# Kernel tuning notes

Measured on AMD Instinct MI355X. Metric: run time of the kernel, lower is better.

## Reference

```python
import jax, jax.numpy as jnp
import numpy as np

T = 2048            # flattened tokens (vLLM style)
D = 4096            # hidden_size
NSSM = 128          # ssm_state_size
K = 4               # conv kernel size
G = 8               # n_groups
H = 128             # mamba_num_heads
P = 64              # mamba_head_dim
INTER = H * P       # 8192 = expand * hidden_size
CONV_DIM = INTER + 2 * G * NSSM   # 10240 (x, B, C share the conv)
PROJ = INTER + CONV_DIM + H       # 18560 (z, xBC, dt)
Q = 128             # SSD chunk size
EPS = 1e-5


def setup_inputs() -> dict:
    key = jax.random.key(0)
    ks = jax.random.split(key, 9)
    s = 0.02
    return {
        "hidden_states": jax.random.normal(ks[0], (T, D), jnp.float32),
        "residual": jax.random.normal(ks[1], (T, D), jnp.float32),
        "norm_w": jnp.ones((D,), jnp.float32),
        "in_proj_w": jax.random.normal(ks[2], (PROJ, D), jnp.float32) * s,
        "conv_w": jax.random.normal(ks[3], (CONV_DIM, K), jnp.float32) * 0.2,
        "conv_b": jax.random.normal(ks[4], (CONV_DIM,), jnp.float32) * 0.1,
        "A_log": jnp.log(jax.random.uniform(ks[5], (H,), jnp.float32, 1.0, 16.0)),
        "D_res": jax.random.normal(ks[6], (H,), jnp.float32) * 0.5 + 1.0,
        "dt_bias": jax.random.normal(ks[7], (H,), jnp.float32) * 0.5,
        "gn_w": jnp.ones((INTER,), jnp.float32),
        "out_proj_w": jax.random.normal(ks[8], (D, INTER), jnp.float32) * s,
    }


def _forward(hidden_states, residual, norm_w, in_proj_w, conv_w, conv_b,
             A_log, D_res, dt_bias, gn_w, out_proj_w):
    # ---- fused add + RMSNorm (vLLM RMSNorm(hidden, residual)) ----
    resid = hidden_states + residual
    hs = resid * jax.lax.rsqrt(jnp.mean(resid * resid, -1, keepdims=True) + EPS) * norm_w

    # ---- MambaMixer2 ----
    proj = hs @ in_proj_w.T                              # [T, PROJ]
    z, xBC, dt = jnp.split(proj, [INTER, INTER + CONV_DIM], axis=-1)

    # causal depthwise conv1d over time + SiLU
    xp = jnp.pad(xBC, ((K - 1, 0), (0, 0)))
    conv = conv_b + sum(conv_w[:, k] * xp[k:k + T] for k in range(K))
    xBC = jax.nn.silu(conv)

    x, B, C = jnp.split(xBC, [INTER, INTER + G * NSSM], axis=-1)
    x = x.reshape(T, H, P)
    Bh = jnp.repeat(B.reshape(T, G, NSSM), H // G, axis=1)   # [T,H,N]
    Ch = jnp.repeat(C.reshape(T, G, NSSM), H // G, axis=1)   # [T,H,N]

    dt = jax.nn.softplus(dt + dt_bias)                   # [T,H]
    A = -jnp.exp(A_log)                                  # [H] (negative)

    # ---- SSD chunked selective scan ----
    NC = T // Q
    a = (dt * A).reshape(NC, Q, H)                       # per-step log decay (<=0)
    cum = jnp.cumsum(a, axis=1)                          # inclusive cumsum, [NC,Q,H]
    Xd = (dt[:, :, None] * x).reshape(NC, Q, H, P)
    Bc = Bh.reshape(NC, Q, H, NSSM)
    Cc = Ch.reshape(NC, Q, H, NSSM)

    # intra-chunk: Y[i] = sum_{j<=i} (C_i.B_j) exp(cum_i-cum_j) Xd_j
    CB = jnp.einsum('cqhn,ckhn->chqk', Cc, Bc)
    cumT = cum.transpose(0, 2, 1)                        # [NC,H,Q]
    mask = jnp.tril(jnp.ones((Q, Q), bool))
    Lm = jnp.where(mask, jnp.exp(cumT[:, :, :, None] - cumT[:, :, None, :]), 0.0)
    Y = jnp.einsum('chqk,ckhp->cqhp', CB * Lm, Xd)

    # chunk-local end states, then scan states across chunks
    cum_end = cum[:, -1]                                 # [NC,H]
    decay_out = jnp.exp(cum_end[:, None] - cum)          # [NC,Q,H]
    S_loc = jnp.einsum('cqhn,cqh,cqhp->chnp', Bc, decay_out, Xd)
    chunk_decay = jnp.exp(cum_end)                       # [NC,H]

    def step(s, inp):
        dec, sl = inp
        return dec[:, None, None] * s + sl, s            # emit state BEFORE chunk

    _, S_prev = jax.lax.scan(step, jnp.zeros((H, NSSM, P), x.dtype),
                             (chunk_decay, S_loc))       # [NC,H,N,P]

    # inter-chunk contribution + skip connection D*x
    Y = Y + jnp.einsum('cqhn,cqh,chnp->cqhp', Cc, jnp.exp(cum), S_prev)
    y = Y.reshape(T, H, P) + D_res[None, :, None] * x

    # gated RMSNorm then out projection
    y = y.reshape(T, INTER) * jax.nn.silu(z)
    y = y * jax.lax.rsqrt(jnp.mean(y * y, -1, keepdims=True) + EPS) * gn_w
    return y @ out_proj_w.T, resid


def reference(hidden_states, residual, norm_w, in_proj_w, conv_w, conv_b,
              A_log, D_res, dt_bias, gn_w, out_proj_w):
    return _forward(hidden_states, residual, norm_w, in_proj_w, conv_w, conv_b,
                    A_log, D_res, dt_bias, gn_w, out_proj_w)
```

## Files before the change

### kernel.cpp

```cpp
#include <hip/hip_runtime.h>
#include <stdint.h>

typedef unsigned short u16;
typedef unsigned int   u32;
typedef float  f32x4  __attribute__((ext_vector_type(4)));
typedef __bf16 bf16x8 __attribute__((ext_vector_type(8)));
typedef u16    u16x4  __attribute__((ext_vector_type(4)));
typedef u16    u16x8  __attribute__((ext_vector_type(8)));

#define T_N     2048
#define D_N     4096
#define H_N     128
#define P_N     64
#define G_N     8
#define NS_N    128
#define INTER_N 8192
#define CONVD_N 10240
#define PROJ_N  18560
#define NGEMM_N 18432
#define NC_N    16

__device__ __forceinline__ float bf2f(u16 u){ u32 x = ((u32)u) << 16; return __builtin_bit_cast(float, x); }
__device__ __forceinline__ u16 f2bf(float f){
  u32 u = __builtin_bit_cast(u32, f);
  u += 0x7FFFu + ((u >> 16) & 1u);
  return (u16)(u >> 16);
}

__device__ __forceinline__ void gld_lds16(const void* g, void* lds){
  __builtin_amdgcn_global_load_lds(
      (const __attribute__((address_space(1))) void*)(uintptr_t)g,
      (__attribute__((address_space(3))) void*)(u32)(uintptr_t)lds,
      16, 0, 0);
}

__global__ __launch_bounds__(256)
void k_addnorm(const float* __restrict__ hin, const float* __restrict__ rin,
               const float* __restrict__ nw, float* __restrict__ resid,
               u16* __restrict__ hs16, float* __restrict__ rstd){
  __shared__ float red[4];
  const int row = blockIdx.x, tid = threadIdx.x;
  const size_t rb = (size_t)row * D_N;
  f32x4 s[4];
  float ss = 0.f;
  #pragma unroll
  for (int i = 0; i < 4; ++i){
    int c4 = tid + i*256;
    f32x4 a = *(const f32x4*)&hin[rb + (size_t)c4*4];
    f32x4 b = *(const f32x4*)&rin[rb + (size_t)c4*4];
    s[i] = a + b;
    *(f32x4*)&resid[rb + (size_t)c4*4] = s[i];
    ss += s[i][0]*s[i][0] + s[i][1]*s[i][1] + s[i][2]*s[i][2] + s[i][3]*s[i][3];
  }
  #pragma unroll
  for (int o = 32; o > 0; o >>= 1) ss += __shfl_down(ss, o, 64);
  if ((tid & 63) == 0) red[tid >> 6] = ss;
  __syncthreads();
  float tot = (red[0] + red[1]) + (red[2] + red[3]);
  float rs = rsqrtf(tot / (float)D_N + 1e-5f);
  if (tid == 0) rstd[row] = rs;
  #pragma unroll
  for (int i = 0; i < 4; ++i){
    int c4 = tid + i*256;
    f32x4 w = *(const f32x4*)&nw[(size_t)c4*4];
    u16x4 o = { f2bf(s[i][0]*rs*w[0]), f2bf(s[i][1]*rs*w[1]),
                f2bf(s[i][2]*rs*w[2]), f2bf(s[i][3]*rs*w[3]) };
    *(u16x4*)&hs16[rb + (size_t)c4*4] = o;
  }
}

__global__ void k_cvt(const float* __restrict__ in, u16* __restrict__ out, size_t n4){
  size_t i = (size_t)blockIdx.x * blockDim.x + threadIdx.x;
  size_t stride = (size_t)gridDim.x * blockDim.x;
  for (; i < n4; i += stride){
    f32x4 v = *(const f32x4*)&in[i*4];
    u16x4 o = { f2bf(v[0]), f2bf(v[1]), f2bf(v[2]), f2bf(v[3]) };
    *(u16x4*)&out[i*4] = o;
  }
}

__global__ __launch_bounds__(256)
void k_wdt(const float* __restrict__ W, const float* __restrict__ nw,
           float* __restrict__ Wn){
  __shared__ float lt[32][133];
  const int tid = threadIdx.x;
  const int d0 = blockIdx.x * 32;
  #pragma unroll
  for (int i = 0; i < 16; ++i){
    int h = i*8 + (tid >> 5);
    int d = tid & 31;
    lt[d][h] = W[(size_t)(INTER_N + CONVD_N + h)*D_N + d0 + d];
  }
  __syncthreads();
  #pragma unroll
  for (int i = 0; i < 4; ++i){
    int d = i*8 + (tid >> 5);
    int h4 = (tid & 31) * 4;
    float nwv = nw[d0 + d];
    f32x4 v = { lt[d][h4]*nwv, lt[d][h4+1]*nwv, lt[d][h4+2]*nwv, lt[d][h4+3]*nwv };
    *(f32x4*)&Wn[(size_t)(d0 + d)*128 + h4] = v;
  }
}

__global__ __launch_bounds__(256)
void k_dtgemm(const float* __restrict__ resid, const float* __restrict__ Wn,
              float* __restrict__ dtpart){
  __shared__ float lhs[16*128];
  const int tid = threadIdx.x;
  const int tb = blockIdx.x >> 3, ks = blockIdx.x & 7;
  const int t0 = tb * 16;
  const int k0 = ks * (D_N / 8);
  const int hcol = tid & 127, rh = tid >> 7;
  float acc[8] = {0,0,0,0,0,0,0,0};
  for (int kt = k0; kt < k0 + D_N/8; kt += 128){
    __syncthreads();
    #pragma unroll
    for (int it = 0; it < 2; ++it){
      int idx = it*256 + tid;
      int rr = idx >> 5, c4 = idx & 31;
      *(f32x4*)&lhs[rr*128 + c4*4] = *(const f32x4*)&resid[(size_t)(t0+rr)*D_N + kt + c4*4];
    }
    __syncthreads();
    #pragma unroll 4
    for (int kk4 = 0; kk4 < 32; ++kk4){
      f32x4 w4;
      #pragma unroll
      for (int j = 0; j < 4; ++j) w4[j] = Wn[(size_t)(kt + kk4*4 + j)*128 + hcol];
      #pragma unroll
      for (int j = 0; j < 8; ++j){
        f32x4 lv = *(const f32x4*)&lhs[(rh*8 + j)*128 + kk4*4];
        acc[j] += lv[0]*w4[0] + lv[1]*w4[1] + lv[2]*w4[2] + lv[3]*w4[3];
      }
    }
  }
  #pragma unroll
  for (int j = 0; j < 8; ++j){
    int t = t0 + rh*8 + j;
    dtpart[((size_t)ks*T_N + t)*128 + hcol] = acc[j];
  }
}

__global__ __launch_bounds__(256)
void k_dtsum(const float* __restrict__ dtpart, const float* __restrict__ rstd,
             const float* __restrict__ dt_bias, const float* __restrict__ A_log,
             float* __restrict__ dtv, float* __restrict__ dta){
  int idx = blockIdx.x*256 + threadIdx.x;
  int t = idx >> 7, h = idx & 127;
  float s = 0.f;
  #pragma unroll
  for (int k = 0; k < 8; ++k) s += dtpart[((size_t)k*T_N + t)*128 + h];
  float x = s * rstd[t] + dt_bias[h];
  float dv = (x > 20.f) ? x : log1pf(expf(x));
  dtv[idx] = dv;
  dta[idx] = dv * (-expf(A_log[h]));
}

__global__ void k_dtprep(const float* __restrict__ dta, float* __restrict__ cum,
                         float* __restrict__ cumend, float* __restrict__ dec){
  int c = blockIdx.x, h = threadIdx.x;
  float cm = 0.f;
  for (int q = 0; q < 128; ++q){
    size_t i = (size_t)(c*128 + q)*128 + h;
    cm += dta[i];
    cum[i] = cm;
  }
  cumend[c*128 + h] = cm;
  dec[c*128 + h] = expf(cm);
}

#define STA(BUF,HH,KT) gld_lds16(pA + (size_t)((HH)*32)*K + (size_t)(KT)*64, shb + (BUF)*BSZ + (HH)*4096 + tid*16)
#define STB(BUF,HH,KT) gld_lds16(pB + (size_t)((HH)*32)*K + (size_t)(KT)*64, shb + (BUF)*BSZ + 16384 + (HH)*4096 + tid*16)
#define VMWN do { asm volatile("s_waitcnt vmcnt(%0)" :: "n"(NF) : "memory"); __builtin_amdgcn_sched_barrier(0); } while(0)
#define RDA4(BUF, MOFF)                                                                 \
    bf16x8 a0 = *(const bf16x8*)(shb + (BUF)*BSZ + rdA + (MOFF)*2048 + sA0);            \
    bf16x8 a1 = *(const bf16x8*)(shb + (BUF)*BSZ + rdA + (MOFF)*2048 + sA1);            \
    bf16x8 a2 = *(const bf16x8*)(shb + (BUF)*BSZ + rdA + ((MOFF)+1)*2048 + sA0);        \
    bf16x8 a3 = *(const bf16x8*)(shb + (BUF)*BSZ + rdA + ((MOFF)+1)*2048 + sA1);
#define RDBALL(BUF, BB)                                                                 \
    _Pragma("unroll") for (int nn = 0; nn < NF; ++nn){                                  \
      BB[nn][0] = *(const bf16x8*)(shb + (BUF)*BSZ + rdB + nn*2048 + sA0);              \
      BB[nn][1] = *(const bf16x8*)(shb + (BUF)*BSZ + rdB + nn*2048 + sA1);              \
    }
#define MM24(MOFF, BB)                                                                  \
    _Pragma("unroll") for (int nn = 0; nn < NF; ++nn)                                   \
      acc[(MOFF)+0][nn] = __builtin_amdgcn_mfma_f32_16x16x32_bf16(a0, BB[nn][0], acc[(MOFF)+0][nn],0,0,0); \
    _Pragma("unroll") for (int nn = 0; nn < NF; ++nn)                                   \
      acc[(MOFF)+1][nn] = __builtin_amdgcn_mfma_f32_16x16x32_bf16(a2, BB[nn][0], acc[(MOFF)+1][nn],0,0,0); \
    _Pragma("unroll") for (int nn = 0; nn < NF; ++nn)                                   \
      acc[(MOFF)+0][nn] = __builtin_amdgcn_mfma_f32_16x16x32_bf16(a1, BB[nn][1], acc[(MOFF)+0][nn],0,0,0); \
    _Pragma("unroll") for (int nn = 0; nn < NF; ++nn)                                   \
      acc[(MOFF)+1][nn] = __builtin_amdgcn_mfma_f32_16x16x32_bf16(a3, BB[nn][1], acc[(MOFF)+1][nn],0,0,0);
#define ENDPH                                                                           \
    __builtin_amdgcn_s_setprio(0);                                                      \
    __builtin_amdgcn_s_barrier();                                                       \
    __builtin_amdgcn_sched_barrier(0);

template<int NF, typename OT>
__global__ __launch_bounds__(256, 2)
void k_gemmw(const u16* __restrict__ A, const u16* __restrict__ Bm,
             OT* __restrict__ C, int ldc, int K, int nkt){
  constexpr int BSZ = 16384 + NF*4096;
  __shared__ char shb[2*BSZ];
  const int tid = threadIdx.x, ln = tid & 63, wid = tid >> 6;
  const int wm = wid >> 1, wn = wid & 1;
  const int lr = ln & 15, lg = ln >> 4;

  const int gx = gridDim.x;
  const int mt = gridDim.y;
  const int lin = blockIdx.y * gx + blockIdx.x;
  const int xcd = lin & 7, sub = lin >> 3;
  const int ncx = gx >> 3;
  const int n_local = sub / mt;
  const int m_idx   = sub % mt;
  const int m0 = m_idx << 7;
  const int n0 = (xcd * ncx + n_local) * (NF*32);

  const int srow = tid >> 3;
  const int slog = ((tid & 7) ^ (srow & 7)) * 8;
  const u16* pA = A + (size_t)(m0 + srow)*K + slog;
  const u16* pB = Bm + (size_t)(n0 + srow)*K + slog;

  const int sA0 = (lg ^ (ln & 7)) << 4;
  const int sA1 = ((4 + lg) ^ (ln & 7)) << 4;
  const u32 rdA = wm*8192 + lr*128;
  const u32 rdB = 16384 + wn*(NF*2048) + lr*128;

  f32x4 acc[4][NF] = {};

  STA(0,0,0); STA(0,1,0); STA(0,2,0); STA(0,3,0);
  #pragma unroll
  for (int hh = 0; hh < NF; ++hh) STB(0, hh, 0);
  #pragma unroll
  for (int hh = 0; hh < NF; ++hh) STB(1, hh, 1);
  VMWN;
  __builtin_amdgcn_s_barrier();
  __builtin_amdgcn_sched_barrier(0);

  const int nit = nkt >> 1;
  #pragma unroll 1
  for (int it = 0; it < nit; ++it){
    const int t1 = 2*it + 1;
    int t2 = 2*it + 2; if (t2 >= nkt) t2 = 0;
    int t3 = 2*it + 3; if (t3 >= nkt) t3 = 1;
    bf16x8 bb0[NF][2], bb1[NF][2];
    { RDA4(0, 0) RDBALL(0, bb0)
      STA(1,0,t1); STA(1,1,t1); STA(1,2,t1); STA(1,3,t1);
      __builtin_amdgcn_s_setprio(1);
      MM24(0, bb0)
      ENDPH }
    { RDA4(0, 2)
      #pragma unroll
      for (int hh = 0; hh < NF; ++hh) STB(0, hh, t2);
      VMWN;
      __builtin_amdgcn_s_setprio(1);
      MM24(2, bb0)
      ENDPH }
    { RDA4(1, 0) RDBALL(1, bb1)
      STA(0,0,t2); STA(0,1,t2); STA(0,2,t2); STA(0,3,t2);
      __builtin_amdgcn_s_setprio(1);
      MM24(0, bb1)
      ENDPH }
    { RDA4(1, 2)
      #pragma unroll
      for (int hh = 0; hh < NF; ++hh) STB(1, hh, t3);
      VMWN;
      __builtin_amdgcn_s_setprio(1);
      MM24(2, bb1)
      ENDPH }
  }
  asm volatile("s_waitcnt vmcnt(0)" ::: "memory");

  const int crow = m0 + wm*64 + lg*4;
  const int ccol = n0 + wn*(NF*16) + lr;
  #pragma unroll
  for (int m = 0; m < 4; ++m)
    #pragma unroll
    for (int nn = 0; nn < NF; ++nn)
      #pragma unroll
      for (int r = 0; r < 4; ++r){
        float v = acc[m][nn][r];
        if constexpr (__is_same(OT, float))
          C[(size_t)(crow + m*16 + r)*ldc + ccol + nn*16] = v;
        else
          C[(size_t)(crow + m*16 + r)*ldc + ccol + nn*16] = f2bf(v);
      }
}

__global__ __launch_bounds__(256)
void k_conv(const u16* __restrict__ proj16, const float* __restrict__ cw,
            const float* __restrict__ cb, u16* __restrict__ x16,
            u16* __restrict__ B16, u16* __restrict__ C16){
  const int ch0 = blockIdx.x*2048 + threadIdx.x*8;
  const int tbase = blockIdx.y*16;
  f32x4 w[8]; float bias[8];
  #pragma unroll
  for (int j = 0; j < 8; ++j){
    w[j] = *(const f32x4*)&cw[(size_t)(ch0+j)*4];
    bias[j] = cb[ch0+j];
  }
  const u16* pcol = proj16 + INTER_N + ch0;
  float p0[8], p1[8], p2[8];
  if (tbase >= 3){
    u16x8 v0 = *(const u16x8*)&pcol[(size_t)(tbase-3)*PROJ_N];
    u16x8 v1 = *(const u16x8*)&pcol[(size_t)(tbase-2)*PROJ_N];
    u16x8 v2 = *(const u16x8*)&pcol[(size_t)(tbase-1)*PROJ_N];
    #pragma unroll
    for (int j = 0; j < 8; ++j){ p0[j]=bf2f(v0[j]); p1[j]=bf2f(v1[j]); p2[j]=bf2f(v2[j]); }
  } else {
    #pragma unroll
    for (int j = 0; j < 8; ++j){ p0[j]=0.f; p1[j]=0.f; p2[j]=0.f; }
  }
  u16* xdst = (ch0 < INTER_N) ? x16 + ch0
            : (ch0 < INTER_N + 1024) ? B16 + (ch0 - INTER_N)
            : C16 + (ch0 - INTER_N - 1024);
  const int dstride = (ch0 < INTER_N) ? INTER_N : 1024;
  #pragma unroll 2
  for (int i = 0; i < 16; ++i){
    int t = tbase + i;
    u16x8 cv = *(const u16x8*)&pcol[(size_t)t*PROJ_N];
    u16x8 o;
    #pragma unroll
    for (int j = 0; j < 8; ++j){
      float cur = bf2f(cv[j]);
      float a = bias[j] + w[j][0]*p0[j] + w[j][1]*p1[j] + w[j][2]*p2[j] + w[j][3]*cur;
      o[j] = f2bf(a / (1.f + __expf(-a)));
      p0[j] = p1[j]; p1[j] = p2[j]; p2[j] = cur;
    }
    *(u16x8*)&xdst[(size_t)t*dstride] = o;
  }
}

__global__ __launch_bounds__(512)
void k_ssda(const u16* __restrict__ B16, const u16* __restrict__ x16,
            const float* __restrict__ dtv, const float* __restrict__ cum,
            const float* __restrict__ cumend, u16* __restrict__ SlocT){
  __shared__ u16 lBdT[128*136];
  __shared__ u16 lXdT[64*136];
  __shared__ float lDec[128], lDt[128];
  const int tid = threadIdx.x, wid = tid >> 6, ln = tid & 63;
  const int c = blockIdx.x >> 7, h = blockIdx.x & 127, g = h >> 4;
  if (tid < 128){
    int t = c*128 + tid;
    lDec[tid] = __expf(cumend[c*128 + h] - cum[(size_t)t*128 + h]);
    lDt[tid]  = dtv[(size_t)t*128 + h];
  }
  __syncthreads();
  for (int it = 0; it < 32; ++it){
    int idx = it*512 + tid;
    int q = idx >> 7, n = idx & 127;
    float bv = bf2f(B16[(size_t)(c*128 + q)*1024 + g*128 + n]) * lDec[q];
    lBdT[n*136 + q] = f2bf(bv);
  }
  for (int it = 0; it < 16; ++it){
    int idx = it*512 + tid;
    int q = idx >> 6, p = idx & 63;
    float xv = bf2f(x16[(size_t)(c*128 + q)*INTER_N + h*64 + p]) * lDt[q];
    lXdT[p*136 + q] = f2bf(xv);
  }
  __syncthreads();
  const int wr = wid >> 1, wc = wid & 1;
  const int kofs = (ln >> 4) << 3;
  f32x4 acc[2][2] = {};
  #pragma unroll
  for (int ks = 0; ks < 4; ++ks){
    bf16x8 a[2], b[2];
    #pragma unroll
    for (int m = 0; m < 2; ++m) a[m] = *(const bf16x8*)&lBdT[(wr*32 + m*16 + (ln & 15))*136 + ks*32 + kofs];
    #pragma unroll
    for (int n = 0; n < 2; ++n) b[n] = *(const bf16x8*)&lXdT[(wc*32 + n*16 + (ln & 15))*136 + ks*32 + kofs];
    #pragma unroll
    for (int m = 0; m < 2; ++m)
      #pragma unroll
      for (int n = 0; n < 2; ++n)
        acc[m][n] = __builtin_amdgcn_mfma_f32_16x16x32_bf16(a[m], b[n], acc[m][n], 0, 0, 0);
  }
  const size_t base = (size_t)(c*128 + h) * 8192;
  #pragma unroll
  for (int m = 0; m < 2; ++m)
    #pragma unroll
    for (int n = 0; n < 2; ++n){
      int p  = wc*32 + n*16 + (ln & 15);
      int nn = wr*32 + m*16 + ((ln >> 4) << 2);
      u16x4 o = { f2bf(acc[m][n][0]), f2bf(acc[m][n][1]), f2bf(acc[m][n][2]), f2bf(acc[m][n][3]) };
      *(u16x4*)&SlocT[base + (size_t)p*128 + nn] = o;
    }
}

__global__ __launch_bounds__(256)
void k_scan(const u16* __restrict__ SlocT, const float* __restrict__ dec,
            u16* __restrict__ SprevT){
  int idx = blockIdx.x*256 + threadIdx.x;
  int h = idx >> 10, p = (idx >> 4) & 63, n8 = (idx & 15)*8;
  float s[8] = {};
  for (int c = 0; c < NC_N; ++c){
    size_t off = (size_t)(c*128 + h)*8192 + (size_t)p*128 + n8;
    u16x8 o;
    #pragma unroll
    for (int j = 0; j < 8; ++j) o[j] = f2bf(s[j]);
    *(u16x8*)&SprevT[off] = o;
    u16x8 sl = *(const u16x8*)&SlocT[off];
    float d = dec[c*128 + h];
    #pragma unroll
    for (int j = 0; j < 8; ++j) s[j] = d*s[j] + bf2f(sl[j]);
  }
}

__global__ __launch_bounds__(512)
void k_ssdb(const u16* __restrict__ C16, const u16* __restrict__ B16g,
            const u16* __restrict__ x16, const float* __restrict__ dtv,
            const float* __restrict__ cum, const u16* __restrict__ SprevT,
            const u16* __restrict__ proj16, const float* __restrict__ Dres,
            u16* __restrict__ yg16){
  __shared__ u16 lC[128*136];
  __shared__ u16 lBP[128*136];
  __shared__ u16 lXdT[64*136];
  __shared__ float lCum[128], lDt[128];
  const int tid = threadIdx.x, wid = tid >> 6, ln = tid & 63;
  const int c = blockIdx.x >> 7, h = blockIdx.x & 127, g = h >> 4;
  if (tid < 128){
    int t = c*128 + tid;
    lCum[tid] = cum[(size_t)t*128 + h];
    lDt[tid]  = dtv[(size_t)t*128 + h];
  }
  __syncthreads();
  #pragma unroll
  for (int it = 0; it < 4; ++it){
    int idx = it*512 + tid;
    int q = idx >> 4, n8 = (idx & 15) << 3;
    size_t gi = (size_t)(c*128 + q)*1024 + g*128 + n8;
    *(u16x8*)&lC[q*136 + n8]  = *(const u16x8*)&C16[gi];
    *(u16x8*)&lBP[q*136 + n8] = *(const u16x8*)&B16g[gi];
  }
  for (int it = 0; it < 16; ++it){
    int idx = it*512 + tid;
    int q = idx >> 6, p = idx & 63;
    lXdT[p*136 + q] = f2bf(bf2f(x16[(size_t)(c*128 + q)*INTER_N + h*64 + p]) * lDt[q]);
  }
  __syncthreads();
  const int kofs = (ln >> 4) << 3;
  {
    const int wr = wid >> 2, wc = wid & 3;
    f32x4 cb[4][2] = {};
    #pragma unroll
    for (int ks = 0; ks < 4; ++ks){
      bf16x8 a[4], b[2];
      #pragma unroll
      for (int m = 0; m < 4; ++m) a[m] = *(const bf16x8*)&lC[(wr*64 + m*16 + (ln & 15))*136 + ks*32 + kofs];
      #pragma unroll
      for (int n = 0; n < 2; ++n) b[n] = *(const bf16x8*)&lBP[(wc*32 + n*16 + (ln & 15))*136 + ks*32 + kofs];
      #pragma unroll
      for (int m = 0; m < 4; ++m)
        #pragma unroll
        for (int n = 0; n < 2; ++n)
          cb[m][n] = __builtin_amdgcn_mfma_f32_16x16x32_bf16(a[m], b[n], cb[m][n], 0, 0, 0);
    }
    __syncthreads();
    #pragma unroll
    for (int m = 0; m < 4; ++m)
      #pragma unroll
      for (int n = 0; n < 2; ++n){
        int kcol = (wid & 3)*32 + n*16 + (ln & 15);
        float ck = lCum[kcol];
        #pragma unroll
        for (int r = 0; r < 4; ++r){
          int q = (wid >> 2)*64 + m*16 + ((ln >> 4) << 2) + r;
          float v = (kcol <= q) ? cb[m][n][r] * __expf(lCum[q] - ck) : 0.f;
          lBP[q*136 + kcol] = f2bf(v);
        }
      }
  }
  __syncthreads();
  const int yr = wid >> 1, yc = wid & 1;
  f32x4 y1[2][2] = {}, y2[2][2] = {};
  const size_t spbase = (size_t)(c*128 + h) * 8192;
  #pragma unroll
  for (int ks = 0; ks < 4; ++ks){
    bf16x8 ap[2], acf[2], bx[2], bs[2];
    #pragma unroll
    for (int m = 0; m < 2; ++m){
      int qr = yr*32 + m*16 + (ln & 15);
      ap[m]  = *(const bf16x8*)&lBP[qr*136 + ks*32 + kofs];
      acf[m] = *(const bf16x8*)&lC [qr*136 + ks*32 + kofs];
    }
    #pragma unroll
    for (int n = 0; n < 2; ++n){
      int p = yc*32 + n*16 + (ln & 15);
      bx[n] = *(const bf16x8*)&lXdT[p*136 + ks*32 + kofs];
      bs[n] = *(const bf16x8*)&SprevT[spbase + (size_t)p*128 + ks*32 + kofs];
    }
    #pragma unroll
    for (int m = 0; m < 2; ++m)
      #pragma unroll
      for (int n = 0; n < 2; ++n){
        y1[m][n] = __builtin_amdgcn_mfma_f32_16x16x32_bf16(ap[m],  bx[n], y1[m][n], 0, 0, 0);
        y2[m][n] = __builtin_amdgcn_mfma_f32_16x16x32_bf16(acf[m], bs[n], y2[m][n], 0, 0, 0);
      }
  }
  const float dh = Dres[h];
  #pragma unroll
  for (int m = 0; m < 2; ++m)
    #pragma unroll
    for (int r = 0; r < 4; ++r){
      int q = yr*32 + m*16 + ((ln >> 4) << 2) + r;
      float eq = __expf(lCum[q]);
      size_t t = (size_t)(c*128 + q);
      #pragma unroll
      for (int n = 0; n < 2; ++n){
        int p = yc*32 + n*16 + (ln & 15);
        int chn = h*64 + p;
        float xv = bf2f(x16[t*INTER_N + chn]);
        float zv = bf2f(proj16[t*PROJ_N + chn]);
        float yv = y1[m][n][r] + eq*y2[m][n][r] + dh*xv;
        float sg = zv / (1.f + __expf(-zv));
        yg16[t*INTER_N + chn] = f2bf(yv * sg);
      }
    }
}

__global__ __launch_bounds__(256)
void k_gnorm(const u16* __restrict__ yg, const float* __restrict__ gnw,
             u16* __restrict__ yn16){
  __shared__ float red[4];
  const int row = blockIdx.x, tid = threadIdx.x;
  const u16* rp = yg + (size_t)row * INTER_N;
  u16x8 v[4];
  float ss = 0.f;
  #pragma unroll
  for (int i = 0; i < 4; ++i){
    v[i] = *(const u16x8*)&rp[(size_t)(tid + i*256)*8];
    #pragma unroll
    for (int j = 0; j < 8; ++j){ float f = bf2f(v[i][j]); ss += f*f; }
  }
  #pragma unroll
  for (int o = 32; o > 0; o >>= 1) ss += __shfl_down(ss, o, 64);
  if ((tid & 63) == 0) red[tid >> 6] = ss;
  __syncthreads();
  float tot = (red[0] + red[1]) + (red[2] + red[3]);
  float sc = rsqrtf(tot / (float)INTER_N + 1e-5f);
  #pragma unroll
  for (int i = 0; i < 4; ++i){
    int c8 = (tid + i*256)*8;
    u16x8 o;
    #pragma unroll
    for (int j = 0; j < 8; ++j)
      o[j] = f2bf(bf2f(v[i][j]) * sc * gnw[c8 + j]);
    *(u16x8*)&yn16[(size_t)row*INTER_N + c8] = o;
  }
}

extern "C" void kernel_launch(void* const* d_in, const int* in_sizes, int n_in,
                              void* d_out, int out_size, void* d_ws, size_t ws_size,
                              hipStream_t stream){
  (void)in_sizes; (void)n_in; (void)out_size;
  const float* hs_in     = (const float*)d_in[0];
  const float* res_in    = (const float*)d_in[1];
  const float* norm_w    = (const float*)d_in[2];
  const float* in_proj_w = (const float*)d_in[3];
  const float* conv_w    = (const float*)d_in[4];
  const float* conv_b    = (const float*)d_in[5];
  const float* A_log     = (const float*)d_in[6];
  const float* D_res     = (const float*)d_in[7];
  const float* dt_bias   = (const float*)d_in[8];
  const float* gn_w      = (const float*)d_in[9];
  const float* out_proj_w= (const float*)d_in[10];

  float* out0      = (float*)d_out;
  float* resid_out = out0 + (size_t)T_N * D_N;

  char* ws = (char*)d_ws;
  const size_t o_hs16   = 0;
  const size_t o_Win16  = 16777216;
  const size_t o_Wout16 = 168820736;
  const size_t o_proj   = 235929600;
  const size_t o_Wn     = 387973120;
  const size_t o_dtv    = 391118848;
  const size_t o_cum    = 392167424;
  const size_t o_cumend = 393216000;
  const size_t o_dec    = 393224192;
  const size_t o_rstd   = 393232384;
  const size_t o_x16    = 393240576;
  const size_t o_B16    = 426795008;
  const size_t o_C16    = 430989312;
  const size_t o_SlocT  = 435183616;
  const size_t o_SprevT = 468738048;
  const size_t o_yn16   = 502292480;
  const size_t WS_NEED  = 535846912;
  if (ws_size < WS_NEED) return;

  u16*   hs16   = (u16*)  (ws + o_hs16);
  u16*   Win16  = (u16*)  (ws + o_Win16);
  u16*   Wout16 = (u16*)  (ws + o_Wout16);
  u16*   proj16 = (u16*)  (ws + o_proj);
  float* Wn     = (float*)(ws + o_Wn);
  float* dtpart = (float*)(ws + o_proj);
  float* dta    = (float*)(ws + o_proj + (16u<<20));
  float* dtv    = (float*)(ws + o_dtv);
  float* cum    = (float*)(ws + o_cum);
  float* cumend = (float*)(ws + o_cumend);
  float* dec    = (float*)(ws + o_dec);
  float* rstd   = (float*)(ws + o_rstd);
  u16*   x16    = (u16*)  (ws + o_x16);
  u16*   B16    = (u16*)  (ws + o_B16);
  u16*   C16    = (u16*)  (ws + o_C16);
  u16*   SlocT  = (u16*)  (ws + o_SlocT);
  u16*   SprevT = (u16*)  (ws + o_SprevT);
  u16*   yn16   = (u16*)  (ws + o_yn16);
  u16*   yg16   = (u16*)  (ws + o_Win16);

  k_addnorm<<<T_N, 256, 0, stream>>>(hs_in, res_in, norm_w, resid_out, hs16, rstd);
  k_cvt<<<4096, 256, 0, stream>>>(in_proj_w,  Win16,  (size_t)NGEMM_N * D_N / 4);
  k_cvt<<<2048, 256, 0, stream>>>(out_proj_w, Wout16, (size_t)D_N * INTER_N / 4);
  k_wdt<<<128, 256, 0, stream>>>(in_proj_w, norm_w, Wn);
  k_dtgemm<<<1024, 256, 0, stream>>>(resid_out, Wn, dtpart);
  k_dtsum<<<1024, 256, 0, stream>>>(dtpart, rstd, dt_bias, A_log, dtv, dta);
  k_dtprep<<<NC_N, 128, 0, stream>>>(dta, cum, cumend, dec);
  k_gemmw<6, u16><<<dim3(NGEMM_N/192, T_N/128), 256, 0, stream>>>(hs16, Win16, proj16, PROJ_N, D_N, D_N/64);
  k_conv<<<dim3(CONVD_N/2048, T_N/16), 256, 0, stream>>>(proj16, conv_w, conv_b, x16, B16, C16);
  k_ssda<<<NC_N * H_N, 512, 0, stream>>>(B16, x16, dtv, cum, cumend, SlocT);
  k_scan<<<512, 256, 0, stream>>>(SlocT, dec, SprevT);
  k_ssdb<<<NC_N * H_N, 512, 0, stream>>>(C16, B16, x16, dtv, cum, SprevT, proj16, D_res, yg16);
  k_gnorm<<<T_N, 256, 0, stream>>>(yg16, gn_w, yn16);
  k_gemmw<4, float><<<dim3(D_N/128, T_N/128), 256, 0, stream>>>(yn16, Wout16, out0, D_N, INTER_N, INTER_N/64);
}
```

Baseline: 802.5 us.

## Add 256x128-tile out-projection GEMM with XCD-aware mapping and merge weight converts

Replaces the out-projection GEMM with a new kernel that uses 256x128 output tiles, 8x4 MFMA fragments per wave, double-buffered LDS with split A/B staging, and a block-to-XCD mapping so neighbouring N tiles share an XCD's L2. The two weight fp32-to-bf16 conversion launches are merged into one kernel. The aim is more data reuse per loaded tile and less launch overhead. The larger tile halves the grid to 256 blocks and uses 96KB of LDS at one block per CU, which may leave some CUs idle.

```diff
diff --git a/kernel.cpp b/kernel.cpp
--- a/kernel.cpp
+++ b/kernel.cpp
@@ -69,13 +69,18 @@
   }
 }
 
-__global__ void k_cvt(const float* __restrict__ in, u16* __restrict__ out, size_t n4){
+__global__ void k_cvt2(const float* __restrict__ in1, u16* __restrict__ out1, size_t n4a,
+                       const float* __restrict__ in2, u16* __restrict__ out2, size_t n4b){
   size_t i = (size_t)blockIdx.x * blockDim.x + threadIdx.x;
   size_t stride = (size_t)gridDim.x * blockDim.x;
-  for (; i < n4; i += stride){
-    f32x4 v = *(const f32x4*)&in[i*4];
+  size_t tot = n4a + n4b;
+  for (; i < tot; i += stride){
+    const float* in = (i < n4a) ? in1 : in2;
+    u16* out = (i < n4a) ? out1 : out2;
+    size_t j = (i < n4a) ? i : i - n4a;
+    f32x4 v = *(const f32x4*)&in[j*4];
     u16x4 o = { f2bf(v[0]), f2bf(v[1]), f2bf(v[2]), f2bf(v[3]) };
-    *(u16x4*)&out[i*4] = o;
+    *(u16x4*)&out[j*4] = o;
   }
 }
 
@@ -284,6 +289,118 @@
         else
           C[(size_t)(crow + m*16 + r)*ldc + ccol + nn*16] = f2bf(v);
       }
+}
+
+#define OSTA(BUF,HH,KT) gld_lds16(qA + (size_t)((HH)*32)*K + (size_t)(KT)*64, shb + (BUF)*49152 + (HH)*4096 + tid*16)
+#define OSTB(BUF,HH,KT) gld_lds16(qB + (size_t)((HH)*32)*K + (size_t)(KT)*64, shb + (BUF)*49152 + 32768 + (HH)*4096 + tid*16)
+#define OVMW do { asm volatile("s_waitcnt vmcnt(4)" ::: "memory"); __builtin_amdgcn_sched_barrier(0); } while(0)
+#define ORDA(BUF, MOFF, AA)                                                             \
+    _Pragma("unroll") for (int mm = 0; mm < 4; ++mm){                                   \
+      AA[mm][0] = *(const bf16x8*)(shb + (BUF)*49152 + rdA + ((MOFF)+mm)*2048 + sA0);   \
+      AA[mm][1] = *(const bf16x8*)(shb + (BUF)*49152 + rdA + ((MOFF)+mm)*2048 + sA1);   \
+    }
+#define ORDB(BUF, BB)                                                                   \
+    _Pragma("unroll") for (int nn = 0; nn < 4; ++nn){                                   \
+      BB[nn][0] = *(const bf16x8*)(shb + (BUF)*49152 + rdB + nn*2048 + sA0);            \
+      BB[nn][1] = *(const bf16x8*)(shb + (BUF)*49152 + rdB + nn*2048 + sA1);            \
+    }
+#define OMM(MOFF, AA, BB)                                                               \
+    _Pragma("unroll") for (int mm = 0; mm < 4; ++mm)                                    \
+      _Pragma("unroll") for (int nn = 0; nn < 4; ++nn)                                  \
+        acc[(MOFF)+mm][nn] = __builtin_amdgcn_mfma_f32_16x16x32_bf16(AA[mm][0], BB[nn][0], acc[(MOFF)+mm][nn],0,0,0); \
+    _Pragma("unroll") for (int mm = 0; mm < 4; ++mm)                                    \
+      _Pragma("unroll") for (int nn = 0; nn < 4; ++nn)                                  \
+        acc[(MOFF)+mm][nn] = __builtin_amdgcn_mfma_f32_16x16x32_bf16(AA[mm][1], BB[nn][1], acc[(MOFF)+mm][nn],0,0,0);
+
+__global__ __launch_bounds__(256, 1)
+void k_gemmo(const u16* __restrict__ A, const u16* __restrict__ Bm,
+             float* __restrict__ C, int ldc, int K, int nkt){
+  __shared__ char shb[98304];
+  const int tid = threadIdx.x, ln = tid & 63, wid = tid >> 6;
+  const int wm = wid >> 1, wn = wid & 1;
+  const int lr = ln & 15, lg = ln >> 4;
+
+  const int gx = gridDim.x;
+  const int mt = gridDim.y;
+  const int lin = blockIdx.y * gx + blockIdx.x;
+  const int xcd = lin & 7, sub = lin >> 3;
+  const int ncx = gx >> 3;
+  const int n_local = sub / mt;
+  const int m_idx   = sub % mt;
+  const int m0 = m_idx << 8;
+  const int n0 = (xcd * ncx + n_local) << 7;
+
+  const int srow = tid >> 3;
+  const int slog = ((tid & 7) ^ (srow & 7)) * 8;
+  const u16* qA = A + (size_t)(m0 + srow)*K + slog;
+  const u16* qB = Bm + (size_t)(n0 + srow)*K + slog;
+
+  const int sA0 = (lg ^ (ln & 7)) << 4;
+  const int sA1 = ((4 + lg) ^ (ln & 7)) << 4;
+  const u32 rdA = wm*16384 + lr*128;
+  const u32 rdB = 32768 + wn*8192 + lr*128;
+
+  f32x4 acc[8][4] = {};
+
+  #pragma unroll
+  for (int hh = 0; hh < 8; ++hh) OSTA(0, hh, 0);
+  #pragma unroll
+  for (int hh = 0; hh < 4; ++hh) OSTB(0, hh, 0);
+  #pragma unroll
+  for (int hh = 0; hh < 4; ++hh) OSTB(1, hh, 1);
+  OVMW;
+  __builtin_amdgcn_s_barrier();
+  __builtin_amdgcn_sched_barrier(0);
+
+  const int nit = nkt >> 1;
+  #pragma unroll 1
+  for (int it = 0; it < nit; ++it){
+    const int t1 = 2*it + 1;
+    int t2 = 2*it + 2; if (t2 >= nkt) t2 = 0;
+    int t3 = 2*it + 3; if (t3 >= nkt) t3 = 1;
+    bf16x8 aa[4][2], bb0[4][2], bb1[4][2];
+    {
+      ORDA(0, 0, aa) ORDB(0, bb0)
+      #pragma unroll
+      for (int hh = 0; hh < 8; ++hh) OSTA(1, hh, t1);
+      __builtin_amdgcn_s_setprio(1);
+      OMM(0, aa, bb0)
+      ENDPH }
+    {
+      ORDA(0, 4, aa)
+      #pragma unroll
+      for (int hh = 0; hh < 4; ++hh) OSTB(0, hh, t2);
+      OVMW;
+      __builtin_amdgcn_s_setprio(1);
+      OMM(4, aa, bb0)
+      ENDPH }
+    {
+      ORDA(1, 0, aa) ORDB(1, bb1)
+      #pragma unroll
+      for (int hh = 0; hh < 8; ++hh) OSTA(0, hh, t2);
+      __builtin_amdgcn_s_setprio(1);
+      OMM(0, aa, bb1)
+      ENDPH }
+    {
+      ORDA(1, 4, aa)
+      #pragma unroll
+      for (int hh = 0; hh < 4; ++hh) OSTB(1, hh, t3);
+      OVMW;
+      __builtin_amdgcn_s_setprio(1);
+      OMM(4, aa, bb1)
+      ENDPH }
+  }
+  asm volatile("s_waitcnt vmcnt(0)" ::: "memory");
+
+  const int crow = m0 + wm*128 + lg*4;
+  const int ccol = n0 + wn*64 + lr;
+  #pragma unroll
+  for (int m = 0; m < 8; ++m)
+    #pragma unroll
+    for (int nn = 0; nn < 4; ++nn)
+      #pragma unroll
+      for (int r = 0; r < 4; ++r)
+        C[(size_t)(crow + m*16 + r)*ldc + ccol + nn*16] = acc[m][nn][r];
 }
 
 __global__ __launch_bounds__(256)
@@ -608,8 +725,8 @@
   u16*   yg16   = (u16*)  (ws + o_Win16);
 
   k_addnorm<<<T_N, 256, 0, stream>>>(hs_in, res_in, norm_w, resid_out, hs16, rstd);
-  k_cvt<<<4096, 256, 0, stream>>>(in_proj_w,  Win16,  (size_t)NGEMM_N * D_N / 4);
-  k_cvt<<<2048, 256, 0, stream>>>(out_proj_w, Wout16, (size_t)D_N * INTER_N / 4);
+  k_cvt2<<<6144, 256, 0, stream>>>(in_proj_w, Win16, (size_t)NGEMM_N * D_N / 4,
+                                   out_proj_w, Wout16, (size_t)D_N * INTER_N / 4);
   k_wdt<<<128, 256, 0, stream>>>(in_proj_w, norm_w, Wn);
   k_dtgemm<<<1024, 256, 0, stream>>>(resid_out, Wn, dtpart);
   k_dtsum<<<1024, 256, 0, stream>>>(dtpart, rstd, dt_bias, A_log, dtv, dta);
@@ -620,5 +737,5 @@
   k_scan<<<512, 256, 0, stream>>>(SlocT, dec, SprevT);
   k_ssdb<<<NC_N * H_N, 512, 0, stream>>>(C16, B16, x16, dtv, cum, SprevT, proj16, D_res, yg16);
   k_gnorm<<<T_N, 256, 0, stream>>>(yg16, gn_w, yn16);
-  k_gemmw<4, float><<<dim3(D_N/128, T_N/128), 256, 0, stream>>>(yn16, Wout16, out0, D_N, INTER_N, INTER_N/64);
-}
+  k_gemmo<<<dim3(D_N/128, T_N/256), 256, 0, stream>>>(yn16, Wout16, out0, D_N, INTER_N, INTER_N/64);
+}
```

Result: slower. 822.9 us, median of 2 (+2.5%).
